# Optimization experiments

Measured on AMD Instinct MI355X. Metric: run time of the kernel, lower is better.

The kernel has to match this reference:

```python
import jax, jax.numpy as jnp
import numpy as np
from jax import lax

B, C, H, W, K = 32, 128, 56, 56, 5
CR = C // 4          # reduced channels in weight-gen MLP
CE = 4 * C           # expanded channels
EPS = 1e-6


def setup_inputs() -> dict:
    key = jax.random.key(0)
    ks = jax.random.split(key, 8)
    s = lambda fan: 1.0 / np.sqrt(fan)
    return {
        "x": jax.random.normal(ks[0], (B, C, H, W), jnp.float32),
        "w_fc1": jax.random.normal(ks[1], (CR, C), jnp.float32) * s(C),
        "ln1_w": jnp.ones((CR,), jnp.float32),
        "ln1_b": jnp.zeros((CR,), jnp.float32),
        "w_fc2": jax.random.normal(ks[2], (C * K * K, CR), jnp.float32) * s(CR),
        "ln2_w": jnp.ones((C,), jnp.float32),
        "ln2_b": jnp.zeros((C,), jnp.float32),
        "w_expand": jax.random.normal(ks[3], (CE, C), jnp.float32) * s(C),
        "w_shrink": jax.random.normal(ks[4], (C, CE), jnp.float32) * s(CE),
        "grn_gamma": jax.random.normal(ks[5], (CE,), jnp.float32) * 0.1,
        "grn_beta": jax.random.normal(ks[6], (CE,), jnp.float32) * 0.1,
    }


def _ln(v, w, b, axis):
    u = v.mean(axis, keepdims=True)
    s2 = jnp.square(v - u).mean(axis, keepdims=True)
    return (v - u) * lax.rsqrt(s2 + EPS) * w + b


def reference(x, w_fc1, ln1_w, ln1_b, w_fc2, ln2_w, ln2_b, w_expand, w_shrink,
              grn_gamma, grn_beta):
    b, c, h, w = x.shape
    # ---- dynamic weight generation: pool -> fc1 -> LN -> fc2 ----
    pooled = x.mean((2, 3))                                  # [B, C]
    hdn = pooled @ w_fc1.T                                   # [B, CR]
    hdn = _ln(hdn, ln1_w, ln1_b, axis=-1)                    # channels_first LN over CR
    dyn = hdn @ w_fc2.T                                      # [B, C*K*K]
    dyn_w = dyn.reshape(b * c, 1, K, K)                      # per-sample depthwise kernels
    # ---- per-sample dynamic depthwise conv (groups = B*C) ----
    pad = K // 2
    out = lax.conv_general_dilated(
        x.reshape(1, b * c, h, w), dyn_w,
        window_strides=(1, 1), padding=[(pad, pad), (pad, pad)],
        dimension_numbers=("NCHW", "OIHW", "NCHW"),
        feature_group_count=b * c,
    ).reshape(b, c, h, w)
    # ---- LN (channels_first) over channel dim ----
    u = out.mean(1, keepdims=True)
    s2 = jnp.square(out - u).mean(1, keepdims=True)
    out = (out - u) * lax.rsqrt(s2 + EPS)
    out = ln2_w[None, :, None, None] * out + ln2_b[None, :, None, None]
    # ---- expand 1x1 -> GELU -> GRN -> shrink 1x1 ----
    out = jnp.einsum("bchw,oc->bohw", out, w_expand)         # [B, 4C, H, W]
    out = jax.nn.gelu(out, approximate=False)
    gx = jnp.sqrt(jnp.sum(jnp.square(out), axis=(2, 3), keepdims=True))  # [B,4C,1,1]
    nx = gx / (gx.mean(1, keepdims=True) + EPS)
    g = grn_gamma[None, :, None, None]
    bt = grn_beta[None, :, None, None]
    out = g * (out * nx) + bt + out
    out = jnp.einsum("bohw,co->bchw", out, w_shrink)         # [B, C, H, W]
    return out + x
```

## Files before the change

### kernel.cpp

```cpp
#include <hip/hip_runtime.h>
#include <hip/hip_bf16.h>

#define B_   32
#define C_   128
#define H_   56
#define W_   56
#define HW_  (H_*W_)
#define BHW_ (B_*HW_)
#define K5_  5
#define KK_  25
#define CR_  32
#define CE_  512
#define EPS_ 1e-6f

typedef __hip_bfloat16 bf16;
typedef __attribute__((ext_vector_type(8))) short short8;
typedef __attribute__((ext_vector_type(4))) float f32x4;


__device__ __forceinline__ float wave_reduce_sum(float v) {
#pragma unroll
  for (int off = 32; off > 0; off >>= 1) v += __shfl_down(v, off, 64);
  return v;
}
__device__ __forceinline__ float bf2f(unsigned short u) {
  return __uint_as_float(((unsigned)u) << 16);
}
__device__ __forceinline__ unsigned short f2bf_bits(float f) {
  bf16 h = __float2bfloat16(f);
  unsigned short u;
  __builtin_memcpy(&u, &h, 2);
  return u;
}
__device__ __forceinline__ float fast_gelu(float v) {
  float t = __expf(-1.702f * v);
  return v * __builtin_amdgcn_rcpf(1.0f + t);
}

__global__ __launch_bounds__(256) void prep_kernel(const float* __restrict__ we,
                                                   const float* __restrict__ ws,
                                                   bf16* __restrict__ weB,
                                                   bf16* __restrict__ wsB) {
  int i = blockIdx.x * 256 + threadIdx.x;
  if (i < CE_ * C_) {
    weB[i] = __float2bfloat16(we[i]);
    wsB[i] = __float2bfloat16(ws[i]);
  }
}

__global__ __launch_bounds__(256) void pool_kernel(const float* __restrict__ x,
                                                   float* __restrict__ pooled) {
  int bc = blockIdx.x;
  const float* xp = x + (size_t)bc * HW_;
  float s = 0.f;
  for (int i = threadIdx.x; i < HW_; i += 256) s += xp[i];
  s = wave_reduce_sum(s);
  __shared__ float red[4];
  int lane = threadIdx.x & 63, wid = threadIdx.x >> 6;
  if (lane == 0) red[wid] = s;
  __syncthreads();
  if (threadIdx.x == 0) pooled[bc] = (red[0] + red[1] + red[2] + red[3]) * (1.0f / HW_);
}

__global__ __launch_bounds__(256) void fc_kernel(const float* __restrict__ pooled,
                                                 const float* __restrict__ w_fc1,
                                                 const float* __restrict__ ln1_w,
                                                 const float* __restrict__ ln1_b,
                                                 const float* __restrict__ w_fc2,
                                                 float* __restrict__ dyn) {
  int b = blockIdx.x;
  int tid = threadIdx.x;
  __shared__ float sp[C_];
  __shared__ float sh[CR_];
  __shared__ float shn[CR_];
  __shared__ float stats[2];
  if (tid < C_) sp[tid] = pooled[b * C_ + tid];
  __syncthreads();
  if (tid < CR_) {
    float acc = 0.f;
    const float* wr = w_fc1 + tid * C_;
#pragma unroll 4
    for (int c = 0; c < C_; ++c) acc += sp[c] * wr[c];
    sh[tid] = acc;
  }
  __syncthreads();
  if (tid == 0) {
    float u = 0.f;
    for (int j = 0; j < CR_; ++j) u += sh[j];
    u *= (1.0f / CR_);
    float v = 0.f;
    for (int j = 0; j < CR_; ++j) { float d = sh[j] - u; v += d * d; }
    v *= (1.0f / CR_);
    stats[0] = u;
    stats[1] = rsqrtf(v + EPS_);
  }
  __syncthreads();
  if (tid < CR_) shn[tid] = (sh[tid] - stats[0]) * stats[1] * ln1_w[tid] + ln1_b[tid];
  __syncthreads();
  for (int i = tid; i < C_ * KK_; i += 256) {
    const float* wr = w_fc2 + i * CR_;
    float acc = 0.f;
#pragma unroll
    for (int j = 0; j < CR_; ++j) acc += shn[j] * wr[j];
    dyn[b * (C_ * KK_) + i] = acc;
  }
}

__global__ __launch_bounds__(256) void conv_kernel(const float* __restrict__ x,
                                                   const float* __restrict__ dyn,
                                                   bf16* __restrict__ z) {
  int bc = blockIdx.x;
  int b = bc >> 7;
  int c = bc & 127;
  int tid = threadIdx.x;
  __shared__ float xs[H_ * 64];
  __shared__ float wks[KK_];
  if (tid < H_ * 4) {
    int r = tid >> 2, q = tid & 3;
    int col = (q < 2) ? q : (56 + q);
    xs[r * 64 + col] = 0.f;
  }
  if (tid < KK_) wks[tid] = dyn[b * (C_ * KK_) + c * KK_ + tid];
  const float4* xp4 = reinterpret_cast<const float4*>(x + (size_t)bc * HW_);
  for (int i = tid; i < 784; i += 256) {
    float4 v = xp4[i];
    int h = i / 14, w4 = (i % 14) * 4;
    float* dst = &xs[h * 64 + 2 + w4];
    dst[0] = v.x; dst[1] = v.y; dst[2] = v.z; dst[3] = v.w;
  }
  __syncthreads();
  float wr[KK_];
#pragma unroll
  for (int j = 0; j < KK_; ++j) wr[j] = wks[j];
  for (int g = tid; g < 784; g += 256) {
    int h = g / 14;
    int w4 = (g % 14) * 4;
    float a0 = 0.f, a1 = 0.f, a2 = 0.f, a3 = 0.f;
#pragma unroll
    for (int dh = 0; dh < K5_; ++dh) {
      int hh = h + dh - 2;
      if (hh < 0 || hh >= H_) continue;
      const float* row = &xs[hh * 64 + w4];
      float4 va = *reinterpret_cast<const float4*>(row);
      float4 vb = *reinterpret_cast<const float4*>(row + 4);
      float v0 = va.x, v1 = va.y, v2 = va.z, v3 = va.w;
      float v4 = vb.x, v5 = vb.y, v6 = vb.z, v7 = vb.w;
      float u0 = wr[dh * 5 + 0], u1 = wr[dh * 5 + 1], u2 = wr[dh * 5 + 2];
      float u3 = wr[dh * 5 + 3], u4 = wr[dh * 5 + 4];
      a0 += v0 * u0 + v1 * u1 + v2 * u2 + v3 * u3 + v4 * u4;
      a1 += v1 * u0 + v2 * u1 + v3 * u2 + v4 * u3 + v5 * u4;
      a2 += v2 * u0 + v3 * u1 + v4 * u2 + v5 * u3 + v6 * u4;
      a3 += v3 * u0 + v4 * u1 + v5 * u2 + v6 * u3 + v7 * u4;
    }
    size_t base = (size_t)bc * HW_ + h * W_ + w4;
    ushort4 pk = make_ushort4(f2bf_bits(a0), f2bf_bits(a1), f2bf_bits(a2), f2bf_bits(a3));
    *reinterpret_cast<ushort4*>(reinterpret_cast<unsigned short*>(z) + base) = pk;
  }
}

__global__ __launch_bounds__(256) void ln_kernel(const bf16* __restrict__ z,
                                                 const float* __restrict__ ln2_w,
                                                 const float* __restrict__ ln2_b,
                                                 bf16* __restrict__ yT) {
  int hw0 = blockIdx.x * 64;
  int b = blockIdx.y;
  int tid = threadIdx.x;
  int wq = tid & 63;
  int cq = tid >> 6;
  __shared__ unsigned short zt[C_][64];
  __shared__ float redS[4][64];
  __shared__ float redQ[4][64];
  __shared__ float meanArr[64];
  __shared__ float invArr[64];
  float s = 0.f, q = 0.f;
  const unsigned short* zp = reinterpret_cast<const unsigned short*>(z);
#pragma unroll 4
  for (int k = 0; k < 32; ++k) {
    int c = cq * 32 + k;
    unsigned short u = zp[((size_t)(b * C_ + c)) * HW_ + hw0 + wq];
    float v = bf2f(u);
    s += v;
    q += v * v;
    zt[c][wq] = u;
  }
  redS[cq][wq] = s;
  redQ[cq][wq] = q;
  __syncthreads();
  if (cq == 0) {
    float ss = redS[0][wq] + redS[1][wq] + redS[2][wq] + redS[3][wq];
    float qq = redQ[0][wq] + redQ[1][wq] + redQ[2][wq] + redQ[3][wq];
    float m = ss * (1.0f / C_);
    float var = qq * (1.0f / C_) - m * m;
    meanArr[wq] = m;
    invArr[wq] = rsqrtf(fmaxf(var, 0.f) + EPS_);
  }
  __syncthreads();
  float m = meanArr[wq], iv = invArr[wq];
  unsigned short* yp =
      reinterpret_cast<unsigned short*>(yT) + ((size_t)(b * HW_ + hw0 + wq)) * C_ + cq * 32;
#pragma unroll
  for (int g = 0; g < 4; ++g) {
    unsigned short pk[8];
#pragma unroll
    for (int i = 0; i < 8; ++i) {
      int c = cq * 32 + g * 8 + i;
      float v = bf2f(zt[c][wq]);
      pk[i] = f2bf_bits((v - m) * iv * ln2_w[c] + ln2_b[c]);
    }
    int4 t;
    __builtin_memcpy(&t, pk, 16);
    *reinterpret_cast<int4*>(yp + g * 8) = t;
  }
}

__global__ __launch_bounds__(256, 4) void expand_mfma(const bf16* __restrict__ yT,
                                                      const bf16* __restrict__ weB,
                                                      bf16* __restrict__ eT,
                                                      float* __restrict__ gx2) {
  int j0 = blockIdx.x * 128;
  int o0 = blockIdx.y * 128;
  int tid = threadIdx.x;
  int lane = tid & 63, wid = tid >> 6;
  int wm = wid >> 1, wn = wid & 1;
  int quad = lane >> 4, l15 = lane & 15;
  __shared__ short As[128][40];
  __shared__ short Bs[128][40];
  f32x4 acc[4][4] = {};
  const short* yTs = reinterpret_cast<const short*>(yT);
  const short* weS = reinterpret_cast<const short*>(weB);
  for (int k0 = 0; k0 < C_; k0 += 32) {
#pragma unroll
    for (int t = tid; t < 512; t += 256) {
      int r = t >> 2, ch = t & 3;
      int4 va = *reinterpret_cast<const int4*>(yTs + (size_t)(j0 + r) * C_ + k0 + ch * 8);
      *reinterpret_cast<int4*>(&As[r][ch * 8]) = va;
      int4 vb = *reinterpret_cast<const int4*>(weS + (size_t)(o0 + r) * C_ + k0 + ch * 8);
      *reinterpret_cast<int4*>(&Bs[r][ch * 8]) = vb;
    }
    __syncthreads();
    short8 a[4], bfr[4];
#pragma unroll
    for (int mf = 0; mf < 4; ++mf)
      a[mf] = *reinterpret_cast<const short8*>(&As[wm * 64 + mf * 16 + l15][quad * 8]);
#pragma unroll
    for (int nf = 0; nf < 4; ++nf)
      bfr[nf] = *reinterpret_cast<const short8*>(&Bs[wn * 64 + nf * 16 + l15][quad * 8]);
#pragma unroll
    for (int mf = 0; mf < 4; ++mf)
#pragma unroll
      for (int nf = 0; nf < 4; ++nf)
        acc[mf][nf] = __builtin_amdgcn_mfma_f32_16x16x32_bf16(a[mf], bfr[nf], acc[mf][nf], 0, 0, 0);
    __syncthreads();
  }
  unsigned short* eP = reinterpret_cast<unsigned short*>(eT);
#pragma unroll
  for (int mf = 0; mf < 4; ++mf) {
    int jm = j0 + wm * 64 + mf * 16;
    int bb = jm / HW_;
    int jb = jm + quad * 4;
#pragma unroll
    for (int nf = 0; nf < 4; ++nf) {
      int o = o0 + wn * 64 + nf * 16 + l15;
      float g2 = 0.f;
#pragma unroll
      for (int r = 0; r < 4; ++r) {
        float ge = fast_gelu(acc[mf][nf][r]);
        g2 += ge * ge;
        eP[(size_t)(jb + r) * CE_ + o] = f2bf_bits(ge);
      }
      g2 += __shfl_xor(g2, 16, 64);
      g2 += __shfl_xor(g2, 32, 64);
      if (quad == 0) atomicAdd(&gx2[bb * CE_ + o], g2);
    }
  }
}

__global__ __launch_bounds__(512) void grn_scale_kernel(const float* __restrict__ gx2,
                                                        const float* __restrict__ gamma,
                                                        float* __restrict__ scale) {
  int b = blockIdx.x;
  int o = threadIdx.x;
  float gx = sqrtf(gx2[b * CE_ + o]);
  float s = wave_reduce_sum(gx);
  __shared__ float red[8];
  __shared__ float meansh;
  int lane = o & 63, wid = o >> 6;
  if (lane == 0) red[wid] = s;
  __syncthreads();
  if (o == 0) {
    float t = 0.f;
    for (int i = 0; i < 8; ++i) t += red[i];
    meansh = t * (1.0f / CE_);
  }
  __syncthreads();
  scale[b * CE_ + o] = 1.0f + gamma[o] * (gx / (meansh + EPS_));
}

__global__ __launch_bounds__(128) void sb_kernel(const float* __restrict__ w_shrink,
                                                 const float* __restrict__ beta,
                                                 float* __restrict__ sb) {
  int c = threadIdx.x;
  float acc = 0.f;
  for (int o = 0; o < CE_; ++o) acc += w_shrink[c * CE_ + o] * beta[o];
  sb[c] = acc;
}

__global__ __launch_bounds__(256) void scale_ws_kernel(const float* __restrict__ ws,
                                                       const float* __restrict__ scale,
                                                       bf16* __restrict__ sws) {
  int c = blockIdx.x;
  int b = blockIdx.y;
  const float* sp = scale + b * CE_;
  const float* wp = ws + (size_t)c * CE_;
  bf16* op = sws + ((size_t)(b * C_ + c)) * CE_;
  for (int i = threadIdx.x; i < CE_; i += 256)
    op[i] = __float2bfloat16(wp[i] * sp[i]);
}

__global__ __launch_bounds__(256, 4) void shrink_mfma(const bf16* __restrict__ eT,
                                                      const bf16* __restrict__ sws,
                                                      const float* __restrict__ sb,
                                                      const float* __restrict__ x,
                                                      float* __restrict__ out) {
  int hw0 = blockIdx.x * 128;
  int b = blockIdx.y;
  int tid = threadIdx.x;
  int lane = tid & 63, wid = tid >> 6;
  int wm = wid >> 1, wn = wid & 1;
  int quad = lane >> 4, l15 = lane & 15;
  __shared__ short As[128][40];
  __shared__ short Bs[128][40];
  f32x4 acc[4][4] = {};
  const short* eS = reinterpret_cast<const short*>(eT) + (size_t)b * HW_ * CE_;
  const short* wsS = reinterpret_cast<const short*>(sws) + (size_t)b * C_ * CE_;
  for (int k0 = 0; k0 < CE_; k0 += 32) {
#pragma unroll
    for (int t = tid; t < 512; t += 256) {
      int r = t >> 2, ch = t & 3;
      int hwc = hw0 + r; if (hwc >= HW_) hwc = HW_ - 1;
      int4 va = *reinterpret_cast<const int4*>(eS + (size_t)hwc * CE_ + k0 + ch * 8);
      *reinterpret_cast<int4*>(&As[r][ch * 8]) = va;
      int4 vb = *reinterpret_cast<const int4*>(wsS + (size_t)r * CE_ + k0 + ch * 8);
      *reinterpret_cast<int4*>(&Bs[r][ch * 8]) = vb;
    }
    __syncthreads();
    short8 a[4], bfr[4];
#pragma unroll
    for (int mf = 0; mf < 4; ++mf)
      a[mf] = *reinterpret_cast<const short8*>(&As[wm * 64 + mf * 16 + l15][quad * 8]);
#pragma unroll
    for (int nf = 0; nf < 4; ++nf)
      bfr[nf] = *reinterpret_cast<const short8*>(&Bs[wn * 64 + nf * 16 + l15][quad * 8]);
#pragma unroll
    for (int mf = 0; mf < 4; ++mf)
#pragma unroll
      for (int nf = 0; nf < 4; ++nf)
        acc[mf][nf] = __builtin_amdgcn_mfma_f32_16x16x32_bf16(a[mf], bfr[nf], acc[mf][nf], 0, 0, 0);
    __syncthreads();
  }
#pragma unroll
  for (int mf = 0; mf < 4; ++mf) {
    int hw = hw0 + wm * 64 + mf * 16 + quad * 4;
    if (hw >= HW_) continue;
#pragma unroll
    for (int nf = 0; nf < 4; ++nf) {
      int c = wn * 64 + nf * 16 + l15;
      size_t base = ((size_t)(b * C_ + c)) * HW_ + hw;
      float add = sb[c];
      float4 xv = *reinterpret_cast<const float4*>(x + base);
      float4 ov;
      ov.x = acc[mf][nf][0] + add + xv.x;
      ov.y = acc[mf][nf][1] + add + xv.y;
      ov.z = acc[mf][nf][2] + add + xv.z;
      ov.w = acc[mf][nf][3] + add + xv.w;
      *reinterpret_cast<float4*>(out + base) = ov;
    }
  }
}

extern "C" void kernel_launch(void* const* d_in, const int* in_sizes, int n_in,
                              void* d_out, int out_size, void* d_ws, size_t ws_size,
                              hipStream_t stream) {
  (void)in_sizes; (void)n_in; (void)out_size; (void)ws_size;
  const float* x        = (const float*)d_in[0];
  const float* w_fc1    = (const float*)d_in[1];
  const float* ln1_w    = (const float*)d_in[2];
  const float* ln1_b    = (const float*)d_in[3];
  const float* w_fc2    = (const float*)d_in[4];
  const float* ln2_w    = (const float*)d_in[5];
  const float* ln2_b    = (const float*)d_in[6];
  const float* w_expand = (const float*)d_in[7];
  const float* w_shrink = (const float*)d_in[8];
  const float* gamma    = (const float*)d_in[9];
  const float* beta     = (const float*)d_in[10];
  float* out = (float*)d_out;

  char* ws = (char*)d_ws;
  float* pooled = (float*)(ws + 0);
  float* dyn    = (float*)(ws + 16384);
  float* gx2    = (float*)(ws + 425984);
  float* scale  = (float*)(ws + 491520);
  float* sb     = (float*)(ws + 557056);
  bf16*  weB    = (bf16*)(ws + 557568);
  bf16*  wsB    = (bf16*)(ws + 688640);
  bf16*  yT     = (bf16*)(ws + 819712);
  bf16*  sws    = (bf16*)(ws + 819712);
  bf16*  eT     = (bf16*)(ws + 26509824);
  bf16*  z      = eT;
  (void)wsB;

  prep_kernel<<<256, 256, 0, stream>>>(w_expand, w_shrink, weB, wsB);
  pool_kernel<<<B_ * C_, 256, 0, stream>>>(x, pooled);
  fc_kernel<<<B_, 256, 0, stream>>>(pooled, w_fc1, ln1_w, ln1_b, w_fc2, dyn);
  conv_kernel<<<B_ * C_, 256, 0, stream>>>(x, dyn, z);
  ln_kernel<<<dim3(49, B_), 256, 0, stream>>>(z, ln2_w, ln2_b, yT);
  hipMemsetAsync(gx2, 0, B_ * CE_ * sizeof(float), stream);
  expand_mfma<<<dim3(784, 4), 256, 0, stream>>>(yT, weB, eT, gx2);
  grn_scale_kernel<<<B_, 512, 0, stream>>>(gx2, gamma, scale);
  sb_kernel<<<1, 128, 0, stream>>>(w_shrink, beta, sb);
  scale_ws_kernel<<<dim3(C_, B_), 256, 0, stream>>>(w_shrink, scale, sws);
  shrink_mfma<<<dim3(25, B_), 256, 0, stream>>>(eT, sws, sb, x, out);
}
```

Baseline: 303.0 us.

## Retile expand/shrink MFMA kernels, coalesce LN stores, pad conv rows, drop unused conversion

Expand GEMM now uses 128x64 tiles with a doubled grid, and the shrink GEMM runs 512-thread blocks (8 waves) with fewer accumulators per wave, both aiming for more waves and occupancy. The LN kernel stages its output in shared memory so each row is written to global memory with coalesced 16-byte stores instead of strided per-thread writes. The conv kernel adds zero padding rows so the inner loop has no boundary branches. The unused w_shrink bf16 conversion is dropped from the prep kernel. The smaller expand tile means more reloads of the activation tile from global memory, and the extra shared buffer in LN can lower occupancy.

```diff
diff --git a/kernel.cpp b/kernel.cpp
--- a/kernel.cpp
+++ b/kernel.cpp
@@ -38,14 +38,9 @@
 }
 
 __global__ __launch_bounds__(256) void prep_kernel(const float* __restrict__ we,
-                                                   const float* __restrict__ ws,
-                                                   bf16* __restrict__ weB,
-                                                   bf16* __restrict__ wsB) {
+                                                   bf16* __restrict__ weB) {
   int i = blockIdx.x * 256 + threadIdx.x;
-  if (i < CE_ * C_) {
-    weB[i] = __float2bfloat16(we[i]);
-    wsB[i] = __float2bfloat16(ws[i]);
-  }
+  if (i < CE_ * C_) weB[i] = __float2bfloat16(we[i]);
 }
 
 __global__ __launch_bounds__(256) void pool_kernel(const float* __restrict__ x,
@@ -113,19 +108,24 @@
   int b = bc >> 7;
   int c = bc & 127;
   int tid = threadIdx.x;
-  __shared__ float xs[H_ * 64];
+  __shared__ float xs[(H_ + 4) * 64];
   __shared__ float wks[KK_];
-  if (tid < H_ * 4) {
+  {
+    int r = tid >> 6;
+    int rr = (r < 2) ? r : (56 + r);
+    xs[rr * 64 + (tid & 63)] = 0.f;
+  }
+  if (tid < 224) {
     int r = tid >> 2, q = tid & 3;
     int col = (q < 2) ? q : (56 + q);
-    xs[r * 64 + col] = 0.f;
+    xs[(r + 2) * 64 + col] = 0.f;
   }
   if (tid < KK_) wks[tid] = dyn[b * (C_ * KK_) + c * KK_ + tid];
   const float4* xp4 = reinterpret_cast<const float4*>(x + (size_t)bc * HW_);
   for (int i = tid; i < 784; i += 256) {
     float4 v = xp4[i];
     int h = i / 14, w4 = (i % 14) * 4;
-    float* dst = &xs[h * 64 + 2 + w4];
+    float* dst = &xs[(h + 2) * 64 + 2 + w4];
     dst[0] = v.x; dst[1] = v.y; dst[2] = v.z; dst[3] = v.w;
   }
   __syncthreads();
@@ -138,9 +138,7 @@
     float a0 = 0.f, a1 = 0.f, a2 = 0.f, a3 = 0.f;
 #pragma unroll
     for (int dh = 0; dh < K5_; ++dh) {
-      int hh = h + dh - 2;
-      if (hh < 0 || hh >= H_) continue;
-      const float* row = &xs[hh * 64 + w4];
+      const float* row = &xs[(h + dh) * 64 + w4];
       float4 va = *reinterpret_cast<const float4*>(row);
       float4 vb = *reinterpret_cast<const float4*>(row + 4);
       float v0 = va.x, v1 = va.y, v2 = va.z, v3 = va.w;
@@ -168,6 +166,7 @@
   int wq = tid & 63;
   int cq = tid >> 6;
   __shared__ unsigned short zt[C_][64];
+  __shared__ unsigned short yt[64][136];
   __shared__ float redS[4][64];
   __shared__ float redQ[4][64];
   __shared__ float meanArr[64];
@@ -196,8 +195,6 @@
   }
   __syncthreads();
   float m = meanArr[wq], iv = invArr[wq];
-  unsigned short* yp =
-      reinterpret_cast<unsigned short*>(yT) + ((size_t)(b * HW_ + hw0 + wq)) * C_ + cq * 32;
 #pragma unroll
   for (int g = 0; g < 4; ++g) {
     unsigned short pk[8];
@@ -209,23 +206,32 @@
     }
     int4 t;
     __builtin_memcpy(&t, pk, 16);
-    *reinterpret_cast<int4*>(yp + g * 8) = t;
-  }
-}
-
-__global__ __launch_bounds__(256, 4) void expand_mfma(const bf16* __restrict__ yT,
+    *reinterpret_cast<int4*>(&yt[wq][cq * 32 + g * 8]) = t;
+  }
+  __syncthreads();
+  unsigned short* yp = reinterpret_cast<unsigned short*>(yT);
+#pragma unroll
+  for (int i = 0; i < 4; ++i) {
+    int t = tid + 256 * i;
+    int row = t >> 4, ch = t & 15;
+    int4 v = *reinterpret_cast<const int4*>(&yt[row][ch * 8]);
+    *reinterpret_cast<int4*>(yp + ((size_t)(b * HW_ + hw0 + row)) * C_ + ch * 8) = v;
+  }
+}
+
+__global__ __launch_bounds__(256, 6) void expand_mfma(const bf16* __restrict__ yT,
                                                       const bf16* __restrict__ weB,
                                                       bf16* __restrict__ eT,
                                                       float* __restrict__ gx2) {
   int j0 = blockIdx.x * 128;
-  int o0 = blockIdx.y * 128;
+  int o0 = blockIdx.y * 64;
   int tid = threadIdx.x;
   int lane = tid & 63, wid = tid >> 6;
   int wm = wid >> 1, wn = wid & 1;
   int quad = lane >> 4, l15 = lane & 15;
   __shared__ short As[128][40];
-  __shared__ short Bs[128][40];
-  f32x4 acc[4][4] = {};
+  __shared__ short Bs[64][40];
+  f32x4 acc[4][2] = {};
   const short* yTs = reinterpret_cast<const short*>(yT);
   const short* weS = reinterpret_cast<const short*>(weB);
   for (int k0 = 0; k0 < C_; k0 += 32) {
@@ -234,21 +240,24 @@
       int r = t >> 2, ch = t & 3;
       int4 va = *reinterpret_cast<const int4*>(yTs + (size_t)(j0 + r) * C_ + k0 + ch * 8);
       *reinterpret_cast<int4*>(&As[r][ch * 8]) = va;
+    }
+    {
+      int r = tid >> 2, ch = tid & 3;
       int4 vb = *reinterpret_cast<const int4*>(weS + (size_t)(o0 + r) * C_ + k0 + ch * 8);
       *reinterpret_cast<int4*>(&Bs[r][ch * 8]) = vb;
     }
     __syncthreads();
-    short8 a[4], bfr[4];
+    short8 a[4], bfr[2];
 #pragma unroll
     for (int mf = 0; mf < 4; ++mf)
       a[mf] = *reinterpret_cast<const short8*>(&As[wm * 64 + mf * 16 + l15][quad * 8]);
 #pragma unroll
-    for (int nf = 0; nf < 4; ++nf)
-      bfr[nf] = *reinterpret_cast<const short8*>(&Bs[wn * 64 + nf * 16 + l15][quad * 8]);
+    for (int nf = 0; nf < 2; ++nf)
+      bfr[nf] = *reinterpret_cast<const short8*>(&Bs[wn * 32 + nf * 16 + l15][quad * 8]);
 #pragma unroll
     for (int mf = 0; mf < 4; ++mf)
 #pragma unroll
-      for (int nf = 0; nf < 4; ++nf)
+      for (int nf = 0; nf < 2; ++nf)
         acc[mf][nf] = __builtin_amdgcn_mfma_f32_16x16x32_bf16(a[mf], bfr[nf], acc[mf][nf], 0, 0, 0);
     __syncthreads();
   }
@@ -259,8 +268,8 @@
     int bb = jm / HW_;
     int jb = jm + quad * 4;
 #pragma unroll
-    for (int nf = 0; nf < 4; ++nf) {
-      int o = o0 + wn * 64 + nf * 16 + l15;
+    for (int nf = 0; nf < 2; ++nf) {
+      int o = o0 + wn * 32 + nf * 16 + l15;
       float g2 = 0.f;
 #pragma unroll
       for (int r = 0; r < 4; ++r) {
@@ -317,7 +326,7 @@
     op[i] = __float2bfloat16(wp[i] * sp[i]);
 }
 
-__global__ __launch_bounds__(256, 4) void shrink_mfma(const bf16* __restrict__ eT,
+__global__ __launch_bounds__(512, 6) void shrink_mfma(const bf16* __restrict__ eT,
                                                       const bf16* __restrict__ sws,
                                                       const float* __restrict__ sb,
                                                       const float* __restrict__ x,
@@ -326,17 +335,17 @@
   int b = blockIdx.y;
   int tid = threadIdx.x;
   int lane = tid & 63, wid = tid >> 6;
-  int wm = wid >> 1, wn = wid & 1;
+  int wm = wid >> 2;
+  int wn = wid & 3;
   int quad = lane >> 4, l15 = lane & 15;
   __shared__ short As[128][40];
   __shared__ short Bs[128][40];
-  f32x4 acc[4][4] = {};
+  f32x4 acc[4][2] = {};
   const short* eS = reinterpret_cast<const short*>(eT) + (size_t)b * HW_ * CE_;
   const short* wsS = reinterpret_cast<const short*>(sws) + (size_t)b * C_ * CE_;
   for (int k0 = 0; k0 < CE_; k0 += 32) {
-#pragma unroll
-    for (int t = tid; t < 512; t += 256) {
-      int r = t >> 2, ch = t & 3;
+    {
+      int r = tid >> 2, ch = tid & 3;
       int hwc = hw0 + r; if (hwc >= HW_) hwc = HW_ - 1;
       int4 va = *reinterpret_cast<const int4*>(eS + (size_t)hwc * CE_ + k0 + ch * 8);
       *reinterpret_cast<int4*>(&As[r][ch * 8]) = va;
@@ -344,36 +353,37 @@
       *reinterpret_cast<int4*>(&Bs[r][ch * 8]) = vb;
     }
     __syncthreads();
-    short8 a[4], bfr[4];
+    short8 a[4], bfr[2];
 #pragma unroll
     for (int mf = 0; mf < 4; ++mf)
       a[mf] = *reinterpret_cast<const short8*>(&As[wm * 64 + mf * 16 + l15][quad * 8]);
 #pragma unroll
-    for (int nf = 0; nf < 4; ++nf)
-      bfr[nf] = *reinterpret_cast<const short8*>(&Bs[wn * 64 + nf * 16 + l15][quad * 8]);
+    for (int nf = 0; nf < 2; ++nf)
+      bfr[nf] = *reinterpret_cast<const short8*>(&Bs[wn * 32 + nf * 16 + l15][quad * 8]);
 #pragma unroll
     for (int mf = 0; mf < 4; ++mf)
 #pragma unroll
-      for (int nf = 0; nf < 4; ++nf)
+      for (int nf = 0; nf < 2; ++nf)
         acc[mf][nf] = __builtin_amdgcn_mfma_f32_16x16x32_bf16(a[mf], bfr[nf], acc[mf][nf], 0, 0, 0);
     __syncthreads();
   }
 #pragma unroll
   for (int mf = 0; mf < 4; ++mf) {
     int hw = hw0 + wm * 64 + mf * 16 + quad * 4;
-    if (hw >= HW_) continue;
-#pragma unroll
-    for (int nf = 0; nf < 4; ++nf) {
-      int c = wn * 64 + nf * 16 + l15;
-      size_t base = ((size_t)(b * C_ + c)) * HW_ + hw;
-      float add = sb[c];
-      float4 xv = *reinterpret_cast<const float4*>(x + base);
-      float4 ov;
-      ov.x = acc[mf][nf][0] + add + xv.x;
-      ov.y = acc[mf][nf][1] + add + xv.y;
-      ov.z = acc[mf][nf][2] + add + xv.z;
-      ov.w = acc[mf][nf][3] + add + xv.w;
-      *reinterpret_cast<float4*>(out + base) = ov;
+    if (hw < HW_) {
+#pragma unroll
+      for (int nf = 0; nf < 2; ++nf) {
+        int c = wn * 32 + nf * 16 + l15;
+        size_t base = ((size_t)(b * C_ + c)) * HW_ + hw;
+        float add = sb[c];
+        float4 xv = *reinterpret_cast<const float4*>(x + base);
+        float4 ov;
+        ov.x = acc[mf][nf][0] + add + xv.x;
+        ov.y = acc[mf][nf][1] + add + xv.y;
+        ov.z = acc[mf][nf][2] + add + xv.z;
+        ov.w = acc[mf][nf][3] + add + xv.w;
+        *reinterpret_cast<float4*>(out + base) = ov;
+      }
     }
   }
 }
@@ -402,22 +412,20 @@
   float* scale  = (float*)(ws + 491520);
   float* sb     = (float*)(ws + 557056);
   bf16*  weB    = (bf16*)(ws + 557568);
-  bf16*  wsB    = (bf16*)(ws + 688640);
   bf16*  yT     = (bf16*)(ws + 819712);
   bf16*  sws    = (bf16*)(ws + 819712);
   bf16*  eT     = (bf16*)(ws + 26509824);
   bf16*  z      = eT;
-  (void)wsB;
-
-  prep_kernel<<<256, 256, 0, stream>>>(w_expand, w_shrink, weB, wsB);
+
+  prep_kernel<<<256, 256, 0, stream>>>(w_expand, weB);
   pool_kernel<<<B_ * C_, 256, 0, stream>>>(x, pooled);
   fc_kernel<<<B_, 256, 0, stream>>>(pooled, w_fc1, ln1_w, ln1_b, w_fc2, dyn);
   conv_kernel<<<B_ * C_, 256, 0, stream>>>(x, dyn, z);
   ln_kernel<<<dim3(49, B_), 256, 0, stream>>>(z, ln2_w, ln2_b, yT);
   hipMemsetAsync(gx2, 0, B_ * CE_ * sizeof(float), stream);
-  expand_mfma<<<dim3(784, 4), 256, 0, stream>>>(yT, weB, eT, gx2);
+  expand_mfma<<<dim3(784, 8), 256, 0, stream>>>(yT, weB, eT, gx2);
   grn_scale_kernel<<<B_, 512, 0, stream>>>(gx2, gamma, scale);
   sb_kernel<<<1, 128, 0, stream>>>(w_shrink, beta, sb);
   scale_ws_kernel<<<dim3(C_, B_), 256, 0, stream>>>(w_shrink, scale, sws);
-  shrink_mfma<<<dim3(25, B_), 256, 0, stream>>>(eT, sws, sb, x, out);
-}
+  shrink_mfma<<<dim3(25, B_), 512, 0, stream>>>(eT, sws, sb, x, out);
+}
```

After: 312.5 us. +3.1%, slower.
